# Performance work log

Hardware: AMD Instinct MI355X
Metric: run time of the kernel (lower is better)

Reference implementation:

```python
import jax, jax.numpy as jnp
import numpy as np

BLOCK_SIZE = 32
# NVFP4 decode table: index bit3 = sign, bits0-2 = magnitude code
DECODE = jnp.array([0.0, 0.5, 1.0, 1.5, 2.0, 3.0, 4.0, 6.0,
                    -0.0, -0.5, -1.0, -1.5, -2.0, -3.0, -4.0, -6.0], dtype=jnp.float32)

N_OUT, K_IN = 16384, 4096


def setup_inputs() -> dict:
    key = jax.random.key(0)
    k1, k2, k3, k4 = jax.random.split(key, 4)
    x = jax.random.normal(k1, (4, 512, K_IN), dtype=jnp.float32)
    # packed uint8 stored as int32 in [0, 256)
    weight_packed = jax.random.randint(k2, (N_OUT, K_IN // 2), 0, 256, dtype=jnp.int32)
    # per-block positive scales (block_max / 6.0 in the original)
    weight_scales = jax.random.uniform(k3, (N_OUT, K_IN // BLOCK_SIZE), dtype=jnp.float32,
                                       minval=1e-3, maxval=5e-2)
    bias = jax.random.normal(k4, (N_OUT,), dtype=jnp.float32) * 0.02
    return {"x": x, "weight_packed": weight_packed, "weight_scales": weight_scales, "bias": bias}


def _dequant(weight_packed, weight_scales):
    # unpack: low nibble -> even K index, high nibble -> odd K index
    low = DECODE[weight_packed & 15]           # [N, K//2]
    high = DECODE[(weight_packed >> 4) & 15]   # [N, K//2]
    n = weight_packed.shape[0]
    w = jnp.stack([low, high], axis=-1).reshape(n, -1)  # [N, K], interleaved
    # expand per-block scales along K
    scales = jnp.repeat(weight_scales, BLOCK_SIZE, axis=1)  # [N, K]
    return w * scales


def reference(x, weight_packed, weight_scales, bias):
    w = _dequant(weight_packed, weight_scales)            # [N, K]
    out = jnp.einsum('bsk,nk->bsn', x, w) + bias          # [B, S, N]
    # activation='gelu' -> F.gelu(approximate='tanh')
    return jax.nn.gelu(out, approximate=True)
```

## Files before the change

### kernel.cpp

```cpp
#include <hip/hip_runtime.h>
#include <hip/hip_bf16.h>

typedef short bf16x8 __attribute__((ext_vector_type(8)));
typedef float f32x4 __attribute__((ext_vector_type(4)));

#define K_DIM 4096
#define N_DIM 16384
#define M_DIM 2048
#define STRIPE 16384
#define TSTRIDE (64 * STRIPE)
#define WSB_BYTES ((size_t)N_DIM * K_DIM * 2)
#define WSA_BYTES ((size_t)M_DIM * K_DIM * 2)

__device__ __forceinline__ unsigned f2bf(float f) {
    unsigned u = __builtin_bit_cast(unsigned, f);
    u += 0x7FFFu + ((u >> 16) & 1u);
    return u >> 16;
}

__device__ __forceinline__ float dec4(unsigned c, float s) {
    unsigned mag = c & 7u;
    unsigned u = (mag >= 2u) ? ((((mag >> 1) + 126u) << 23) | ((mag & 1u) << 22))
                             : (mag == 1u ? 0x3F000000u : 0u);
    u |= (c & 8u) << 28;
    return __builtin_bit_cast(float, u) * s;
}

__device__ __forceinline__ float gelu_tanh(float v) {
    float c = v + 0.044715f * v * v * v;
    float t = tanhf(0.7978845608028654f * c);
    return 0.5f * v * (1.0f + t);
}

__global__ __launch_bounds__(256) void dequant_w(const int* __restrict__ wp,
                                                 const float* __restrict__ wsc,
                                                 unsigned char* __restrict__ dst) {
    int t = blockIdx.x * 256 + threadIdx.x;
    int n = t >> 9;
    int ck = t & 511;
    int kstep = ck >> 3, s = ck & 7;
    int nt = n >> 7, r = n & 127;

    const int4 p4 = *reinterpret_cast<const int4*>(wp + (size_t)n * (K_DIM / 2) + kstep * 32 + s * 4);
    float scale = wsc[(size_t)n * (K_DIM / 32) + kstep * 2 + (s >> 2)];

    const int pv[4] = {p4.x, p4.y, p4.z, p4.w};
    unsigned o[8];
    #pragma unroll
    for (int j = 0; j < 4; ++j) {
        unsigned b = (unsigned)pv[j] & 255u;
        o[2 * j]     = f2bf(dec4(b & 15u, scale));
        o[2 * j + 1] = f2bf(dec4((b >> 4) & 15u, scale));
    }
    uint4 v;
    v.x = o[0] | (o[1] << 16);
    v.y = o[2] | (o[3] << 16);
    v.z = o[4] | (o[5] << 16);
    v.w = o[6] | (o[7] << 16);

    size_t off = (size_t)(nt * 64 + kstep) * STRIPE
               + (size_t)r * 128 + (size_t)((s ^ (r & 7)) << 4);
    *reinterpret_cast<uint4*>(dst + off) = v;
}

__global__ __launch_bounds__(256) void conv_x(const float* __restrict__ x,
                                              unsigned char* __restrict__ dst) {
    int t = blockIdx.x * 256 + threadIdx.x;
    int m = t >> 9;
    int ck = t & 511;
    int kstep = ck >> 3, s = ck & 7;
    int mt = m >> 7, r = m & 127;

    const float4* xp = reinterpret_cast<const float4*>(x + (size_t)m * K_DIM + kstep * 64 + s * 8);
    float4 a = xp[0], b = xp[1];
    uint4 v;
    v.x = f2bf(a.x) | (f2bf(a.y) << 16);
    v.y = f2bf(a.z) | (f2bf(a.w) << 16);
    v.z = f2bf(b.x) | (f2bf(b.y) << 16);
    v.w = f2bf(b.z) | (f2bf(b.w) << 16);

    size_t off = (size_t)(mt * 64 + kstep) * STRIPE
               + (size_t)r * 128 + (size_t)((s ^ (r & 7)) << 4);
    *reinterpret_cast<uint4*>(dst + off) = v;
}


__global__ __launch_bounds__(512, 2) void gemm_bf16_256(
    const unsigned char* __restrict__ wsA,
    const unsigned char* __restrict__ wsB,
    const float* __restrict__ bias,
    float* __restrict__ out)
{
    __shared__ unsigned char lds[131072];

    int id = blockIdx.x;
    int wg = (id & 7) * 64 + (id >> 3);
    int MT = wg & 7;
    int NT = wg >> 3;

    const int tid  = threadIdx.x;
    const int lane = tid & 63;
    const int w    = tid >> 6;
    const int wm   = w >> 2;
    const int wn   = w & 3;
    const int fr   = lane & 15;
    const int fg   = lane >> 4;

    const unsigned char* gA = wsA + (size_t)(2 * MT) * TSTRIDE;
    const unsigned char* gB = wsB + (size_t)(2 * NT) * TSTRIDE;

    int addrA[8];
    #pragma unroll
    for (int mi = 0; mi < 8; ++mi) {
        int row = wm * 128 + mi * 16 + fr;
        int L = row >> 1;
        addrA[mi] = L * 128 + (((((row & 1) << 2) | fg) ^ (L & 7)) << 4);
    }
    int addrB[4];
    #pragma unroll
    for (int ni = 0; ni < 4; ++ni) {
        int row = wn * 64 + ni * 16 + fr;
        int L = row >> 1;
        addrB[ni] = L * 128 + (((((row & 1) << 2) | fg) ^ (L & 7)) << 4);
    }

    int offST[2][2];
    #pragma unroll
    for (int j = 0; j < 2; ++j) {
        int c = w * 2 + j;
        int L = c * 8 + (lane >> 3);
        int p = lane & 7;
        int sl = p ^ (L & 7);
        int h = sl >> 2, fgs = sl & 3;
        int row = 2 * L + h;
        #pragma unroll
        for (int kb = 0; kb < 2; ++kb)
            offST[j][kb] = (row >> 7) * TSTRIDE + (row & 127) * 128
                         + ((((kb << 2) | fgs) ^ (row & 7)) << 4);
    }

#define GLDS(SRC, DOFF) __builtin_amdgcn_global_load_lds(                          \
        (const __attribute__((address_space(1))) unsigned int*)(SRC),              \
        (__attribute__((address_space(3))) unsigned int*)(&lds[DOFF]), 16, 0, 0)

#define STAGE_A(KSOFF, KB, SLOT) do {                                              \
        GLDS(gA + (KSOFF) + offST[0][KB], ((SLOT) << 14) + (w * 2 + 0) * 1024);    \
        GLDS(gA + (KSOFF) + offST[1][KB], ((SLOT) << 14) + (w * 2 + 1) * 1024);    \
    } while (0)
#define STAGE_B(KSOFF, KB, SLOT) do {                                              \
        GLDS(gB + (KSOFF) + offST[0][KB], 65536 + ((SLOT) << 14) + (w * 2 + 0) * 1024); \
        GLDS(gB + (KSOFF) + offST[1][KB], 65536 + ((SLOT) << 14) + (w * 2 + 1) * 1024); \
    } while (0)

#define READ_PF(PA, PB, SLOT) do {                                                 \
        const unsigned char* La_ = lds + ((SLOT) << 14);                           \
        const unsigned char* Lb_ = lds + 65536 + ((SLOT) << 14);                   \
        _Pragma("unroll") for (int ni = 0; ni < 4; ++ni)                           \
            PB[ni] = *reinterpret_cast<const bf16x8*>(Lb_ + addrB[ni]);            \
        _Pragma("unroll") for (int mi = 0; mi < 4; ++mi)                           \
            PA[mi] = *reinterpret_cast<const bf16x8*>(La_ + addrA[mi]);            \
    } while (0)

    f32x4 acc[8][4];
    #pragma unroll
    for (int mi = 0; mi < 8; ++mi)
        #pragma unroll
        for (int ni = 0; ni < 4; ++ni)
            acc[mi][ni] = (f32x4){0.f, 0.f, 0.f, 0.f};

    bf16x8 pa0[4], pb0[4], pa1[4], pb1[4];

    STAGE_A(0, 0, 0);        STAGE_B(0, 0, 0);
    STAGE_A(0, 1, 1);        STAGE_B(0, 1, 1);
    STAGE_A(STRIPE, 0, 2);   STAGE_B(STRIPE, 0, 2);
    asm volatile("s_waitcnt vmcnt(4)" ::: "memory");
    __builtin_amdgcn_sched_barrier(0);
    __builtin_amdgcn_s_barrier();
    __builtin_amdgcn_sched_barrier(0);
    READ_PF(pa0, pb0, 0);

#define TILE_BODY(RSLOT, NSLOT, PA, PB, NPA, NPB, DO_STG, STKS, STKB, SSLOT, DO_PF, VMN) do { \
        const unsigned char* la = lds + ((RSLOT) << 14);                           \
        bf16x8 ka[4];                                                              \
        if (DO_STG) STAGE_A(STKS, STKB, SSLOT);                                    \
        _Pragma("unroll") for (int mi = 0; mi < 4; ++mi)                           \
            ka[mi] = *reinterpret_cast<const bf16x8*>(la + addrA[4 + mi]);         \
        __builtin_amdgcn_s_setprio(1);                                             \
        _Pragma("unroll") for (int mi = 0; mi < 4; ++mi)                           \
            _Pragma("unroll") for (int ni = 0; ni < 4; ++ni)                       \
                acc[mi][ni] = __builtin_amdgcn_mfma_f32_16x16x32_bf16(             \
                    PA[mi], PB[ni], acc[mi][ni], 0, 0, 0);                         \
        __builtin_amdgcn_s_setprio(0);                                             \
        if (DO_STG) STAGE_B(STKS, STKB, SSLOT);                                    \
        if (DO_PF) READ_PF(NPA, NPB, NSLOT);                                       \
        __builtin_amdgcn_s_setprio(1);                                             \
        _Pragma("unroll") for (int mi = 0; mi < 4; ++mi)                           \
            _Pragma("unroll") for (int ni = 0; ni < 4; ++ni)                       \
                acc[4 + mi][ni] = __builtin_amdgcn_mfma_f32_16x16x32_bf16(         \
                    ka[mi], PB[ni], acc[4 + mi][ni], 0, 0, 0);                     \
        __builtin_amdgcn_s_setprio(0);                                             \
        if ((VMN) >= 0) {                                                          \
            if ((VMN) == 4)      asm volatile("s_waitcnt vmcnt(4)" ::: "memory");  \
            else                 asm volatile("s_waitcnt vmcnt(0)" ::: "memory");  \
            __builtin_amdgcn_sched_barrier(0);                                     \
            __builtin_amdgcn_s_barrier();                                          \
            __builtin_amdgcn_sched_barrier(0);                                     \
        }                                                                          \
    } while (0)

    for (int tp = 0; tp < 62; ++tp) {
        const int scur = (tp & 1) << 1;
        const int ks1 = (tp + 1) * STRIPE;
        const int ks2 = (tp + 2) * STRIPE;
        TILE_BODY(scur,     scur ^ 1, pa0, pb0, pa1, pb1, 1, ks1, 1, scur ^ 3, 1, 4);
        TILE_BODY(scur ^ 1, scur ^ 2, pa1, pb1, pa0, pb0, 1, ks2, 0, scur,     1, 4);
    }
    TILE_BODY(0, 1, pa0, pb0, pa1, pb1, 1, 63 * STRIPE, 1, 3, 1, 4);
    TILE_BODY(1, 2, pa1, pb1, pa0, pb0, 0, 0, 0, 0, 1, 0);
    TILE_BODY(2, 3, pa0, pb0, pa1, pb1, 0, 0, 0, 0, 1, 0);
    TILE_BODY(3, 0, pa1, pb1, pa0, pb0, 0, 0, 0, 0, 0, -1);

    const int bm0 = MT * 256, bn0 = NT * 256;
    #pragma unroll
    for (int mi = 0; mi < 8; ++mi) {
        int row = bm0 + wm * 128 + mi * 16 + fg * 4;
        #pragma unroll
        for (int ni = 0; ni < 4; ++ni) {
            int col = bn0 + wn * 64 + ni * 16 + fr;
            float bv = bias[col];
            float* op = out + (size_t)row * N_DIM + col;
            #pragma unroll
            for (int q = 0; q < 4; ++q) {
                float v = acc[mi][ni][q] + bv;
                op[(size_t)q * N_DIM] = gelu_tanh(v);
            }
        }
    }
#undef TILE_BODY
#undef READ_PF
#undef STAGE_A
#undef STAGE_B
#undef GLDS
}

__global__ __launch_bounds__(256, 2) void nvfp4_gemm(
    const float* __restrict__ x,
    const int*   __restrict__ wp,
    const float* __restrict__ wscale,
    const float* __restrict__ bias,
    float* __restrict__ out)
{
    __shared__ uint4  lsA[128 * 8];
    __shared__ uint4  lsB[128 * 8];
    __shared__ float2 lut[256];

    const int tid = threadIdx.x;
    {
        static const float dectab[16] = {0.f, 0.5f, 1.f, 1.5f, 2.f, 3.f, 4.f, 6.f,
                                         -0.f,-0.5f,-1.f,-1.5f,-2.f,-3.f,-4.f,-6.f};
        lut[tid] = make_float2(dectab[tid & 15], dectab[(tid >> 4) & 15]);
    }

    const int bn0 = blockIdx.x * 128;
    const int bm0 = blockIdx.y * 128;
    const int r = tid >> 1;
    const int h = tid & 1;

    const float4* xp = reinterpret_cast<const float4*>(x + (size_t)(bm0 + r) * K_DIM) + h * 8;
    const uint4*  bp = reinterpret_cast<const uint4*>(wp + (size_t)(bn0 + r) * (K_DIM / 2)) + h * 4;
    const float*  sp = wscale + (size_t)(bn0 + r) * (K_DIM / 32) + h;

    float4 ax[8];
    uint4  bx[4];
    float  scale;
    #pragma unroll
    for (int j = 0; j < 8; ++j) ax[j] = xp[j];
    #pragma unroll
    for (int q = 0; q < 4; ++q) bx[q] = bp[q];
    scale = sp[0];

    f32x4 acc[4][4];
    #pragma unroll
    for (int mi = 0; mi < 4; ++mi)
        #pragma unroll
        for (int ni = 0; ni < 4; ++ni)
            acc[mi][ni] = (f32x4){0.f, 0.f, 0.f, 0.f};

    const int lane = tid & 63;
    const int wid  = tid >> 6;
    const int wm0  = (wid >> 1) * 64;
    const int wn0  = (wid & 1) * 64;
    const int fr   = lane & 15;
    const int fg   = lane >> 4;

    __syncthreads();

    for (int kt = 0; kt < 64; ++kt) {
        #pragma unroll
        for (int j = 0; j < 4; ++j) {
            float4 f0 = ax[2 * j], f1 = ax[2 * j + 1];
            uint4 v;
            v.x = f2bf(f0.x) | (f2bf(f0.y) << 16);
            v.y = f2bf(f0.z) | (f2bf(f0.w) << 16);
            v.z = f2bf(f1.x) | (f2bf(f1.y) << 16);
            v.w = f2bf(f1.z) | (f2bf(f1.w) << 16);
            lsA[(r * 8 + h * 4 + j) ^ (r & 7)] = v;
        }
        #pragma unroll
        for (int q = 0; q < 4; ++q) {
            uint4 p = bx[q];
            float2 d0 = lut[p.x & 255];
            float2 d1 = lut[p.y & 255];
            float2 d2 = lut[p.z & 255];
            float2 d3 = lut[p.w & 255];
            uint4 v;
            v.x = f2bf(d0.x * scale) | (f2bf(d0.y * scale) << 16);
            v.y = f2bf(d1.x * scale) | (f2bf(d1.y * scale) << 16);
            v.z = f2bf(d2.x * scale) | (f2bf(d2.y * scale) << 16);
            v.w = f2bf(d3.x * scale) | (f2bf(d3.y * scale) << 16);
            lsB[(r * 8 + h * 4 + q) ^ (r & 7)] = v;
        }
        __syncthreads();

        if (kt + 1 < 64) {
            #pragma unroll
            for (int j = 0; j < 8; ++j) ax[j] = xp[(kt + 1) * 16 + j];
            #pragma unroll
            for (int q = 0; q < 4; ++q) bx[q] = bp[(kt + 1) * 8 + q];
            scale = sp[(kt + 1) * 2];
        }

        #pragma unroll
        for (int kk = 0; kk < 2; ++kk) {
            bf16x8 af[4], bfr[4];
            #pragma unroll
            for (int mi = 0; mi < 4; ++mi) {
                int row = wm0 + mi * 16 + fr;
                af[mi] = __builtin_bit_cast(bf16x8, lsA[(row * 8 + kk * 4 + fg) ^ (row & 7)]);
            }
            #pragma unroll
            for (int ni = 0; ni < 4; ++ni) {
                int row = wn0 + ni * 16 + fr;
                bfr[ni] = __builtin_bit_cast(bf16x8, lsB[(row * 8 + kk * 4 + fg) ^ (row & 7)]);
            }
            #pragma unroll
            for (int mi = 0; mi < 4; ++mi)
                #pragma unroll
                for (int ni = 0; ni < 4; ++ni)
                    acc[mi][ni] = __builtin_amdgcn_mfma_f32_16x16x32_bf16(
                        af[mi], bfr[ni], acc[mi][ni], 0, 0, 0);
        }
        __syncthreads();
    }

    #pragma unroll
    for (int mi = 0; mi < 4; ++mi) {
        int row = bm0 + wm0 + mi * 16 + fg * 4;
        #pragma unroll
        for (int ni = 0; ni < 4; ++ni) {
            int col = bn0 + wn0 + ni * 16 + fr;
            float bv = bias[col];
            float* op = out + (size_t)row * N_DIM + col;
            #pragma unroll
            for (int q = 0; q < 4; ++q) {
                float v = acc[mi][ni][q] + bv;
                op[(size_t)q * N_DIM] = gelu_tanh(v);
            }
        }
    }
}

extern "C" void kernel_launch(void* const* d_in, const int* in_sizes, int n_in,
                              void* d_out, int out_size, void* d_ws, size_t ws_size,
                              hipStream_t stream) {
    const float* x    = (const float*)d_in[0];
    const int*   wp   = (const int*)d_in[1];
    const float* wsc  = (const float*)d_in[2];
    const float* bias = (const float*)d_in[3];
    float*       out  = (float*)d_out;
    (void)in_sizes; (void)n_in; (void)out_size;

    if (ws_size >= WSB_BYTES + WSA_BYTES) {
        unsigned char* wsB = (unsigned char*)d_ws;
        unsigned char* wsA = wsB + WSB_BYTES;
        dequant_w<<<(N_DIM * (K_DIM / 8)) / 256, 256, 0, stream>>>(wp, wsc, wsB);
        conv_x<<<(M_DIM * (K_DIM / 8)) / 256, 256, 0, stream>>>(x, wsA);
        gemm_bf16_256<<<(M_DIM / 256) * (N_DIM / 256), 512, 0, stream>>>(wsA, wsB, bias, out);
    } else {
        dim3 grid(N_DIM / 128, M_DIM / 128);
        nvfp4_gemm<<<grid, 256, 0, stream>>>(x, wp, wsc, bias, out);
    }
}
```

Before: 319.8 us.

## Load B operand fragments directly from global into registers, bypassing LDS

```diff
diff --git a/kernel.cpp b/kernel.cpp
--- a/kernel.cpp
+++ b/kernel.cpp
@@ -91,7 +91,7 @@
     const float* __restrict__ bias,
     float* __restrict__ out)
 {
-    __shared__ unsigned char lds[131072];
+    __shared__ unsigned char lds[65536];
 
     int id = blockIdx.x;
     int wg = (id & 7) * 64 + (id >> 3);
@@ -116,13 +116,15 @@
         int L = row >> 1;
         addrA[mi] = L * 128 + (((((row & 1) << 2) | fg) ^ (L & 7)) << 4);
     }
-    int addrB[4];
-    #pragma unroll
-    for (int ni = 0; ni < 4; ++ni) {
-        int row = wn * 64 + ni * 16 + fr;
-        int L = row >> 1;
-        addrB[ni] = L * 128 + (((((row & 1) << 2) | fg) ^ (L & 7)) << 4);
-    }
+    int offBG[2][4];
+    #pragma unroll
+    for (int kb = 0; kb < 2; ++kb)
+        #pragma unroll
+        for (int ni = 0; ni < 4; ++ni) {
+            int row = wn * 64 + ni * 16 + fr;
+            offBG[kb][ni] = (row >> 7) * TSTRIDE + (row & 127) * 128
+                          + ((((kb << 2) | fg) ^ (row & 7)) << 4);
+        }
 
     int offST[2][2];
     #pragma unroll
@@ -147,16 +149,9 @@
         GLDS(gA + (KSOFF) + offST[0][KB], ((SLOT) << 14) + (w * 2 + 0) * 1024);    \
         GLDS(gA + (KSOFF) + offST[1][KB], ((SLOT) << 14) + (w * 2 + 1) * 1024);    \
     } while (0)
-#define STAGE_B(KSOFF, KB, SLOT) do {                                              \
-        GLDS(gB + (KSOFF) + offST[0][KB], 65536 + ((SLOT) << 14) + (w * 2 + 0) * 1024); \
-        GLDS(gB + (KSOFF) + offST[1][KB], 65536 + ((SLOT) << 14) + (w * 2 + 1) * 1024); \
-    } while (0)
-
-#define READ_PF(PA, PB, SLOT) do {                                                 \
+
+#define READ_PFA(PA, SLOT) do {                                                    \
         const unsigned char* La_ = lds + ((SLOT) << 14);                           \
-        const unsigned char* Lb_ = lds + 65536 + ((SLOT) << 14);                   \
-        _Pragma("unroll") for (int ni = 0; ni < 4; ++ni)                           \
-            PB[ni] = *reinterpret_cast<const bf16x8*>(Lb_ + addrB[ni]);            \
         _Pragma("unroll") for (int mi = 0; mi < 4; ++mi)                           \
             PA[mi] = *reinterpret_cast<const bf16x8*>(La_ + addrA[mi]);            \
     } while (0)
@@ -168,21 +163,30 @@
         for (int ni = 0; ni < 4; ++ni)
             acc[mi][ni] = (f32x4){0.f, 0.f, 0.f, 0.f};
 
-    bf16x8 pa0[4], pb0[4], pa1[4], pb1[4];
-
-    STAGE_A(0, 0, 0);        STAGE_B(0, 0, 0);
-    STAGE_A(0, 1, 1);        STAGE_B(0, 1, 1);
-    STAGE_A(STRIPE, 0, 2);   STAGE_B(STRIPE, 0, 2);
-    asm volatile("s_waitcnt vmcnt(4)" ::: "memory");
+    bf16x8 pa0[4], pa1[4];
+    bf16x8 pb0[4], pb1[4];
+
+    #pragma unroll
+    for (int ni = 0; ni < 4; ++ni)
+        pb0[ni] = *reinterpret_cast<const bf16x8*>(gB + offBG[0][ni]);
+    __builtin_amdgcn_sched_barrier(0);
+    STAGE_A(0, 0, 0);        STAGE_A(0, 1, 1);        STAGE_A(STRIPE, 0, 2);
+    __builtin_amdgcn_sched_barrier(0);
+    asm volatile("s_waitcnt vmcnt(2)" ::: "memory");
     __builtin_amdgcn_sched_barrier(0);
     __builtin_amdgcn_s_barrier();
     __builtin_amdgcn_sched_barrier(0);
-    READ_PF(pa0, pb0, 0);
-
-#define TILE_BODY(RSLOT, NSLOT, PA, PB, NPA, NPB, DO_STG, STKS, STKB, SSLOT, DO_PF, VMN) do { \
+    READ_PFA(pa0, 0);
+
+#define TILE_BODY(RSLOT, NSLOT, PA, PB, NPA, NPB, DO_STG, STKS, STKB, SSLOT, DO_PF, DO_B, BBASE, BKB, VMN) do { \
         const unsigned char* la = lds + ((RSLOT) << 14);                           \
         bf16x8 ka[4];                                                              \
-        if (DO_STG) STAGE_A(STKS, STKB, SSLOT);                                    \
+        if (DO_B) {                                                                \
+            _Pragma("unroll") for (int ni = 0; ni < 4; ++ni)                       \
+                NPB[ni] = *reinterpret_cast<const bf16x8*>((BBASE) + offBG[BKB][ni]); \
+            __builtin_amdgcn_sched_barrier(0);                                     \
+        }                                                                          \
+        if (DO_STG) { STAGE_A(STKS, STKB, SSLOT); __builtin_amdgcn_sched_barrier(0); } \
         _Pragma("unroll") for (int mi = 0; mi < 4; ++mi)                           \
             ka[mi] = *reinterpret_cast<const bf16x8*>(la + addrA[4 + mi]);         \
         __builtin_amdgcn_s_setprio(1);                                             \
@@ -191,8 +195,7 @@
                 acc[mi][ni] = __builtin_amdgcn_mfma_f32_16x16x32_bf16(             \
                     PA[mi], PB[ni], acc[mi][ni], 0, 0, 0);                         \
         __builtin_amdgcn_s_setprio(0);                                             \
-        if (DO_STG) STAGE_B(STKS, STKB, SSLOT);                                    \
-        if (DO_PF) READ_PF(NPA, NPB, NSLOT);                                       \
+        if (DO_PF) READ_PFA(NPA, NSLOT);                                           \
         __builtin_amdgcn_s_setprio(1);                                             \
         _Pragma("unroll") for (int mi = 0; mi < 4; ++mi)                           \
             _Pragma("unroll") for (int ni = 0; ni < 4; ++ni)                       \
@@ -200,7 +203,7 @@
                     ka[mi], PB[ni], acc[4 + mi][ni], 0, 0, 0);                     \
         __builtin_amdgcn_s_setprio(0);                                             \
         if ((VMN) >= 0) {                                                          \
-            if ((VMN) == 4)      asm volatile("s_waitcnt vmcnt(4)" ::: "memory");  \
+            if ((VMN) == 2)      asm volatile("s_waitcnt vmcnt(2)" ::: "memory");  \
             else                 asm volatile("s_waitcnt vmcnt(0)" ::: "memory");  \
             __builtin_amdgcn_sched_barrier(0);                                     \
             __builtin_amdgcn_s_barrier();                                          \
@@ -212,13 +215,15 @@
         const int scur = (tp & 1) << 1;
         const int ks1 = (tp + 1) * STRIPE;
         const int ks2 = (tp + 2) * STRIPE;
-        TILE_BODY(scur,     scur ^ 1, pa0, pb0, pa1, pb1, 1, ks1, 1, scur ^ 3, 1, 4);
-        TILE_BODY(scur ^ 1, scur ^ 2, pa1, pb1, pa0, pb0, 1, ks2, 0, scur,     1, 4);
-    }
-    TILE_BODY(0, 1, pa0, pb0, pa1, pb1, 1, 63 * STRIPE, 1, 3, 1, 4);
-    TILE_BODY(1, 2, pa1, pb1, pa0, pb0, 0, 0, 0, 0, 1, 0);
-    TILE_BODY(2, 3, pa0, pb0, pa1, pb1, 0, 0, 0, 0, 1, 0);
-    TILE_BODY(3, 0, pa1, pb1, pa0, pb0, 0, 0, 0, 0, 0, -1);
+        const unsigned char* bB1 = gB + (size_t)tp * STRIPE;
+        const unsigned char* bB2 = gB + (size_t)(tp + 1) * STRIPE;
+        TILE_BODY(scur,     scur ^ 1, pa0, pb0, pa1, pb1, 1, ks1, 1, scur ^ 3, 1, 1, bB1, 1, 2);
+        TILE_BODY(scur ^ 1, scur ^ 2, pa1, pb1, pa0, pb0, 1, ks2, 0, scur,     1, 1, bB2, 0, 2);
+    }
+    TILE_BODY(0, 1, pa0, pb0, pa1, pb1, 1, 63 * STRIPE, 1, 3, 1, 1, gB + 62 * STRIPE, 1, 2);
+    TILE_BODY(1, 2, pa1, pb1, pa0, pb0, 0, 0, 0, 0, 1, 1, gB + 63 * STRIPE, 0, 0);
+    TILE_BODY(2, 3, pa0, pb0, pa1, pb1, 0, 0, 0, 0, 1, 1, gB + 63 * STRIPE, 1, 0);
+    TILE_BODY(3, 0, pa1, pb1, pa0, pb0, 0, 0, 0, 0, 0, 0, gB, 0, -1);
 
     const int bm0 = MT * 256, bn0 = NT * 256;
     #pragma unroll
@@ -237,9 +242,8 @@
         }
     }
 #undef TILE_BODY
-#undef READ_PF
+#undef READ_PFA
 #undef STAGE_A
-#undef STAGE_B
 #undef GLDS
 }
 
@@ -388,6 +392,6 @@
         gemm_bf16_256<<<(M_DIM / 256) * (N_DIM / 256), 512, 0, stream>>>(wsA, wsB, bias, out);
     } else {
         dim3 grid(N_DIM / 128, M_DIM / 128);
-        nvfp4_gemm<<<grid, 256, 0, stream>>>(x, wp, wsc, bias, out);
-    }
-}
+        nvfp4_gemm<<<grid, 128 * 2, 0, stream>>>(x, wp, wsc, bias, out);
+    }
+}
```

Result: slower. 412.2 us (+28.9%).
